# Optimization experiments

Hardware: AMD Instinct MI355X
Metric: run time of the kernel (lower is better)

The kernel has to match this reference:

```python
import jax, jax.numpy as jnp
import numpy as np
from jax import lax

BN_EPS = 1e-5


def _bn(t, g, b, m, v):
    # eval-mode BatchNorm2d over channel axis 1
    scale = (g / jnp.sqrt(v + BN_EPS))[None, :, None, None]
    return (t - m[None, :, None, None]) * scale + b[None, :, None, None]


def _conv1x1(t, w):
    # w: (out_c, in_c)
    return jnp.einsum('bchw,oc->bohw', t, w)


def setup_inputs() -> dict:
    key = jax.random.key(0)
    ks = jax.random.split(key, 8)
    B, C_in, H, W = 16, 640, 32, 32
    x = jax.random.normal(ks[0], (B, C_in, H, W), dtype=jnp.float32)

    def bn_params(k, c):
        k1, k2, k3, k4 = jax.random.split(k, 4)
        return (jax.random.normal(k1, (c,), jnp.float32) * 0.1 + 1.0,  # gamma
                jax.random.normal(k2, (c,), jnp.float32) * 0.1,        # beta
                jax.random.normal(k3, (c,), jnp.float32) * 0.1,        # running mean
                jax.random.uniform(k4, (c,), jnp.float32) + 0.5)       # running var

    bn1_g, bn1_b, bn1_m, bn1_v = bn_params(ks[1], 640)
    w_in = jax.random.normal(ks[2], (64, 640), jnp.float32) / np.sqrt(640)
    bnin_g, bnin_b, bnin_m, bnin_v = bn_params(ks[3], 64)
    w_emb = jax.random.normal(ks[4], (640, 1664), jnp.float32) / np.sqrt(1664)
    bne_g, bne_b, bne_m, bne_v = bn_params(ks[5], 640)
    w_out = jax.random.normal(ks[6], (640, 640), jnp.float32) / np.sqrt(640)
    bno_g, bno_b, bno_m, bno_v = bn_params(ks[7], 640)

    return dict(x=x,
                bn1_g=bn1_g, bn1_b=bn1_b, bn1_m=bn1_m, bn1_v=bn1_v,
                w_in=w_in, bnin_g=bnin_g, bnin_b=bnin_b, bnin_m=bnin_m, bnin_v=bnin_v,
                w_emb=w_emb, bne_g=bne_g, bne_b=bne_b, bne_m=bne_m, bne_v=bne_v,
                w_out=w_out, bno_g=bno_g, bno_b=bno_b, bno_m=bno_m, bno_v=bno_v)


def reference(x,
              bn1_g, bn1_b, bn1_m, bn1_v,
              w_in, bnin_g, bnin_b, bnin_m, bnin_v,
              w_emb, bne_g, bne_b, bne_m, bne_v,
              w_out, bno_g, bno_b, bno_m, bno_v):
    KH, KW = 5, 5
    x = jax.nn.relu(_bn(x, bn1_g, bn1_b, bn1_m, bn1_v))
    x = jax.nn.relu(_bn(_conv1x1(x, w_in), bnin_g, bnin_b, bnin_m, bnin_v))
    x0 = jax.nn.relu(x)  # second ReLU in original forward (no-op but faithful)
    # F.normalize(x, dim=1, p=2), eps=1e-12 (PyTorch default)
    norm = jnp.sqrt(jnp.sum(x0 * x0, axis=1, keepdims=True))
    identity = x0 / jnp.maximum(norm, 1e-12)
    b, c, h, w = identity.shape
    # unfold: (b, c*KH*KW, h, w), channel-major ordering matches torch Unfold
    patches = lax.conv_general_dilated_patches(
        identity, (KH, KW), (1, 1), ((2, 2), (2, 2)))
    corr = patches.reshape(b, c, KH * KW, h, w) * identity[:, :, None, :, :]
    corr = corr.reshape(b, c * KH * KW, h, w)
    # featureL2Norm: sqrt(sum(x^2, 1) + 1e-6)
    gs = corr / jnp.sqrt(jnp.sum(corr * corr, axis=1, keepdims=True) + 1e-6)
    feat = jnp.concatenate([identity, gs], axis=1)  # (b, 1664, h, w)
    e = jax.nn.relu(_bn(_conv1x1(feat, w_emb), bne_g, bne_b, bne_m, bne_v))
    out = _bn(_conv1x1(e, w_out), bno_g, bno_b, bno_m, bno_v)
    # dropout in eval mode = identity
    return out
```

## Files before the change

kernel.cpp:

```cpp
#include <hip/hip_runtime.h>
#include <math.h>

#define BN_EPS 1e-5f

using short8  = __attribute__((ext_vector_type(8))) short;
using f32x16  = __attribute__((ext_vector_type(16))) float;


__device__ __forceinline__ float bflo(unsigned u) { return __uint_as_float(u << 16); }
__device__ __forceinline__ float bfhi(unsigned u) { return __uint_as_float(u & 0xffff0000u); }

__device__ __forceinline__ unsigned bf16_rne(float f) {
    unsigned u = __float_as_uint(f);
    return (u + 0x7fffu + ((u >> 16) & 1u)) >> 16;
}
__device__ __forceinline__ unsigned pack_bf16(float lo, float hi) {
    return bf16_rne(lo) | (bf16_rne(hi) << 16);
}
__device__ __forceinline__ unsigned pk_hu(float lo, float hi) {
    unsigned a = __float_as_uint(lo) + 0x8000u;
    unsigned b = __float_as_uint(hi) + 0x8000u;
    return __builtin_amdgcn_perm(b, a, 0x07060302u);
}
__device__ __forceinline__ unsigned pmul_fast(unsigned a, unsigned b) {
    return pk_hu(bflo(a) * bflo(b), bfhi(a) * bfhi(b));
}

__global__ __launch_bounds__(256)
void k_prepAll(const float* __restrict__ g1, const float* __restrict__ b1,
               const float* __restrict__ m1, const float* __restrict__ v1,
               const float* __restrict__ w_in,
               const float* __restrict__ gi, const float* __restrict__ bi,
               const float* __restrict__ mi, const float* __restrict__ vi,
               const float* __restrict__ w_emb,
               const float* __restrict__ ge, const float* __restrict__ be,
               const float* __restrict__ me, const float* __restrict__ ve,
               const float* __restrict__ w_out,
               const float* __restrict__ go, const float* __restrict__ bo,
               const float* __restrict__ mo, const float* __restrict__ vo,
               float* __restrict__ s1, float* __restrict__ b1c,
               float* __restrict__ biasI, float* __restrict__ biasE, float* __restrict__ biasO,
               unsigned* __restrict__ wIt, unsigned* __restrict__ wEt, unsigned* __restrict__ wOt)
{
    __shared__ float row[1664];
    const int tid = threadIdx.x;

    if (blockIdx.x < 640) {
        const int oc = blockIdx.x;
#pragma unroll
        for (int it = 0; it < 2; it++) {
            int u = it * 256 + tid;
            if (u < 416)
                ((float4*)row)[u] = ((const float4*)&w_emb[(size_t)oc * 1664])[u];
        }
        __syncthreads();
        if (tid < 208) {
            int kc = tid >> 2, kh = (tid >> 1) & 1, ksub = tid & 1;
            int k0 = kc * 32 + kh * 16 + ksub * 8;
            float sc = ge[oc] * rsqrtf(ve[oc] + BN_EPS);
            float v[8];
#pragma unroll
            for (int j = 0; j < 8; j++) {
                int kgp = k0 + j;
                int orig;
                if (kgp < 64) orig = kgp;
                else { int t = kgp - 64; orig = 64 + (t & 63) * 25 + (t >> 6); }
                v[j] = row[orig] * sc;
            }
            int mt = oc >> 7, mf = (oc >> 5) & 3;
            int idx = (mt * 52 + kc) * 512 + (mf * 2 + kh) * 64 + ksub * 32 + (oc & 31);
            ((uint4*)wEt)[idx] = make_uint4(pack_bf16(v[0], v[1]), pack_bf16(v[2], v[3]),
                                            pack_bf16(v[4], v[5]), pack_bf16(v[6], v[7]));
        }
        return;
    }

    int i = (blockIdx.x - 640) * 256 + tid;

    if (i < 640) {
        float s = g1[i] * rsqrtf(v1[i] + BN_EPS);
        s1[i] = s; b1c[i] = b1[i] - m1[i] * s;
    } else if (i < 704) {
        int c = i - 640;
        float s = gi[c] * rsqrtf(vi[c] + BN_EPS);
        biasI[c] = bi[c] - mi[c] * s;
    } else if (i < 1344) {
        int c = i - 704;
        float s = ge[c] * rsqrtf(ve[c] + BN_EPS);
        biasE[c] = be[c] - me[c] * s;
    } else if (i < 1984) {
        int c = i - 1344;
        float s = go[c] * rsqrtf(vo[c] + BN_EPS);
        biasO[c] = bo[c] - mo[c] * s;
    }

    if (i >= 2048 && i < 7168) {
        int u = i - 2048;
        int kc = u >> 8, w = u & 255;
        int mf = w >> 7, kh = (w >> 6) & 1, sl = w & 63;
        int oc = mf * 32 + (sl & 31);
        int k0 = kc * 32 + kh * 16 + (sl >> 5) * 8;
        float sc = gi[oc] * rsqrtf(vi[oc] + BN_EPS);
        unsigned d[4];
#pragma unroll
        for (int q = 0; q < 4; q++)
            d[q] = pack_bf16(w_in[oc * 640 + k0 + 2 * q] * sc,
                             w_in[oc * 640 + k0 + 2 * q + 1] * sc);
        ((uint4*)wIt)[u] = make_uint4(d[0], d[1], d[2], d[3]);
    }

    if (i >= 8192 && i < 59392) {
        int u = i - 8192;
        int ci = u >> 9, w = u & 511;
        int mt = ci / 20, kc = ci - mt * 20;
        int mf = w >> 7, kh = (w >> 6) & 1, sl = w & 63;
        int oc = mt * 128 + mf * 32 + (sl & 31);
        int k0 = kc * 32 + kh * 16 + (sl >> 5) * 8;
        float sc = go[oc] * rsqrtf(vo[oc] + BN_EPS);
        unsigned d[4];
#pragma unroll
        for (int q = 0; q < 4; q++)
            d[q] = pack_bf16(w_out[oc * 640 + k0 + 2 * q] * sc,
                             w_out[oc * 640 + k0 + 2 * q + 1] * sc);
        ((uint4*)wOt)[u] = make_uint4(d[0], d[1], d[2], d[3]);
    }
}

__global__ __launch_bounds__(512, 1)
void k_identity(const float* __restrict__ x,
                const float* __restrict__ s1, const float* __restrict__ b1c,
                const unsigned* __restrict__ wIt, const float* __restrict__ biasI,
                unsigned* __restrict__ ident)
{
    __shared__ short smem[2][4096];
    __shared__ float Tpart[64 * 65];
    __shared__ float T[64 * 68];
    __shared__ float inv[64];

    const int tid  = threadIdx.x;
    const int half = tid >> 8;
    const int t    = tid & 255;
    const int l = t & 63, wv = t >> 6;
    const int mf = wv >> 1, nf = wv & 1;
    const int p0 = blockIdx.x * 64;
    const int b = p0 >> 10, hw0 = p0 & 1023;

    f32x16 acc;
#pragma unroll
    for (int r = 0; r < 16; r++) acc[r] = 0.f;

    for (int i = 0; i < 10; i++) {
        const int kc = half * 10 + i;
        uint4 av = ((const uint4*)wIt)[kc * 256 + t];
        int bnf = t >> 7, bkh = (t >> 6) & 1, sl = t & 63;
        int px = bnf * 32 + (sl & 31);
        int ch0 = kc * 32 + bkh * 16 + (sl >> 5) * 8;
        float4 sA = *(const float4*)&s1[ch0], sB = *(const float4*)&s1[ch0 + 4];
        float4 bA = *(const float4*)&b1c[ch0], bB = *(const float4*)&b1c[ch0 + 4];
        float vv[8];
        const float* xp = &x[((size_t)b * 640 + ch0) * 1024 + hw0 + px];
        vv[0] = fmaxf(fmaf(xp[0], sA.x, bA.x), 0.f);
        vv[1] = fmaxf(fmaf(xp[1024], sA.y, bA.y), 0.f);
        vv[2] = fmaxf(fmaf(xp[2048], sA.z, bA.z), 0.f);
        vv[3] = fmaxf(fmaf(xp[3072], sA.w, bA.w), 0.f);
        vv[4] = fmaxf(fmaf(xp[4096], sB.x, bB.x), 0.f);
        vv[5] = fmaxf(fmaf(xp[5120], sB.y, bB.y), 0.f);
        vv[6] = fmaxf(fmaf(xp[6144], sB.z, bB.z), 0.f);
        vv[7] = fmaxf(fmaf(xp[7168], sB.w, bB.w), 0.f);
        uint4 bvpk = make_uint4(pack_bf16(vv[0], vv[1]), pack_bf16(vv[2], vv[3]),
                                pack_bf16(vv[4], vv[5]), pack_bf16(vv[6], vv[7]));
        __syncthreads();
        ((uint4*)smem[half])[t] = av;
        ((uint4*)(smem[half] + 2048))[t] = bvpk;
        __syncthreads();
#pragma unroll
        for (int kh = 0; kh < 2; kh++) {
            short8 a  = *(const short8*)&smem[half][((mf * 2 + kh) * 64 + l) * 8];
            short8 bb = *(const short8*)&smem[half][2048 + ((nf * 2 + kh) * 64 + l) * 8];
            acc = __builtin_amdgcn_mfma_f32_32x32x16_bf16(a, bb, acc, 0, 0, 0);
        }
    }
    if (half == 1) {
#pragma unroll
        for (int r = 0; r < 16; r++) {
            int m = mf * 32 + (r & 3) + 8 * (r >> 2) + 4 * (l >> 5);
            int px = nf * 32 + (l & 31);
            Tpart[px * 65 + m] = acc[r];
        }
    }
    __syncthreads();
    if (half == 0) {
#pragma unroll
        for (int r = 0; r < 16; r++) {
            int m = mf * 32 + (r & 3) + 8 * (r >> 2) + 4 * (l >> 5);
            int px = nf * 32 + (l & 31);
            float v = acc[r] + Tpart[px * 65 + m];
            T[px * 68 + m] = fmaxf(v + biasI[m], 0.f);
        }
    }
    __syncthreads();
    if (tid < 64) {
        float sum = 0.f;
#pragma unroll 8
        for (int c = 0; c < 64; c++) { float v = T[tid * 68 + c]; sum = fmaf(v, v, sum); }
        inv[tid] = 1.f / fmaxf(sqrtf(sum), 1e-12f);
    }
    __syncthreads();
    {
        int px = tid >> 3, q = tid & 7;
        float iv = inv[px];
        unsigned d[4];
#pragma unroll
        for (int t2 = 0; t2 < 4; t2++)
            d[t2] = pack_bf16(T[px * 68 + q * 8 + 2 * t2] * iv,
                              T[px * 68 + q * 8 + 2 * t2 + 1] * iv);
        *(uint4*)&ident[(size_t)(p0 + px) * 32 + q * 4] = make_uint4(d[0], d[1], d[2], d[3]);
    }
}

#define FS_SLAB 0
#define FS_CTRS 15552
__global__ __launch_bounds__(512, 1)
void k_feat(const unsigned* __restrict__ ident, unsigned* __restrict__ featC, int ptBase)
{
    __shared__ short smem[20160];
    __shared__ float invDs[64];

    const int tid = threadIdx.x;
    const int pt = ptBase + blockIdx.x;
    const int b = pt >> 4, r0 = (pt & 15) * 2;

#pragma unroll
    for (int it = 0; it < 4; it++) {
        int u = it * 512 + tid;
        if (u < 1728) {
            int spx = u >> 3, q = u & 7;
            int sr = spx / 36, sc = spx - sr * 36;
            int r = r0 + sr - 2, c = sc - 2;
            uint4 v = make_uint4(0u, 0u, 0u, 0u);
            if (r >= 0 && r < 32 && c >= 0 && c < 32)
                v = *(const uint4*)&ident[((size_t)(b * 1024 + r * 32 + c) * 64 + q * 8) / 2];
            *(uint4*)&smem[FS_SLAB + spx * 72 + q * 8] = v;
        }
    }
    __syncthreads();

    {
        int px = tid >> 3, part = tid & 7;
        int rh = px >> 5, rw = px & 31;
        float ctr[8];
        const unsigned* cp = (const unsigned*)&smem[FS_SLAB + ((rh + 2) * 36 + rw + 2) * 72 + part * 8];
#pragma unroll
        for (int d = 0; d < 4; d++) { ctr[2 * d] = bflo(cp[d]); ctr[2 * d + 1] = bfhi(cp[d]); }
        float sum = 0.f;
#pragma unroll
        for (int k = 0; k < 25; k++) {
            const int kh = k / 5, kw = k % 5;
            const unsigned* nb = (const unsigned*)&smem[FS_SLAB + ((rh + kh) * 36 + rw + kw) * 72 + part * 8];
#pragma unroll
            for (int d = 0; d < 4; d++) {
                float q0 = bflo(nb[d]) * ctr[2 * d];
                float q1 = bfhi(nb[d]) * ctr[2 * d + 1];
                sum = fmaf(q0, q0, sum); sum = fmaf(q1, q1, sum);
            }
        }
        sum += __shfl_xor(sum, 1);
        sum += __shfl_xor(sum, 2);
        sum += __shfl_xor(sum, 4);
        if (part == 0) invDs[px] = rsqrtf(sum + 1e-6f);
    }
    __syncthreads();

    {
        int px = tid >> 3, q = tid & 7;
        int spx = ((px >> 5) + 2) * 36 + (px & 31) + 2;
        const unsigned* src = (const unsigned*)&smem[FS_SLAB + spx * 72 + q * 8];
        float iv = invDs[px];
        unsigned d[4];
#pragma unroll
        for (int dd = 0; dd < 4; dd++)
            d[dd] = pk_hu(bflo(src[dd]) * iv, bfhi(src[dd]) * iv);
        *(uint4*)&smem[FS_CTRS + px * 72 + q * 8] = make_uint4(d[0], d[1], d[2], d[3]);
    }
    __syncthreads();

    const int t = tid & 255;
    const int hf = t >> 7, bkh = (t >> 6) & 1, sl = t & 63;
    const int pxl = hf * 32 + (sl & 31);
    const int cl = bkh * 16 + (sl >> 5) * 8;
    const int spxC = (hf + 2) * 36 + (sl & 31) + 2;
    const int kcH = tid >> 8;
    uint4* dst = (uint4*)featC + (size_t)blockIdx.x * 52 * 256 + t;

    for (int it = 0; it < 26; it++) {
        int kc = it * 2 + kcH;
        uint4 f;
        if (kc < 2) {
            f = *(const uint4*)&smem[FS_SLAB + spxC * 72 + kc * 32 + cl];
        } else {
            int idx = kc - 2;
            int ksp = idx >> 1;
            int cb = (idx & 1) * 32 + cl;
            int kho = ksp / 5, kwo = ksp - kho * 5;
            int spx = (hf + kho) * 36 + (sl & 31) + kwo;
            const unsigned* nb = (const unsigned*)&smem[FS_SLAB + spx * 72 + cb];
            const unsigned* ct = (const unsigned*)&smem[FS_CTRS + pxl * 72 + cb];
            f = make_uint4(pmul_fast(nb[0], ct[0]), pmul_fast(nb[1], ct[1]),
                           pmul_fast(nb[2], ct[2]), pmul_fast(nb[3], ct[3]));
        }
        dst[kc * 256] = f;
    }
}

__global__ __launch_bounds__(128, 3)
void k_emb(const unsigned* __restrict__ featC, const unsigned* __restrict__ wEt,
           const float* __restrict__ biasE, unsigned* __restrict__ eG, int ntBase)
{
    __shared__ short Ep[64 * 136];

    const int tid = threadIdx.x;
    const int l = tid & 63, mh = tid >> 6;
    const int ntL = blockIdx.x, mt = blockIdx.y;

    f32x16 acc[2][2];
#pragma unroll
    for (int i = 0; i < 2; i++)
#pragma unroll
        for (int j = 0; j < 2; j++)
#pragma unroll
            for (int r = 0; r < 16; r++) acc[i][j][r] = 0.f;

    const uint4* A = (const uint4*)wEt + (size_t)(mt * 52) * 512;
    const uint4* B = (const uint4*)featC + (size_t)ntL * 52 * 256;

    for (int kc = 0; kc < 52; kc++) {
        uint4 av[2][2], bv[2][2];
#pragma unroll
        for (int mi = 0; mi < 2; mi++)
#pragma unroll
            for (int kh = 0; kh < 2; kh++)
                av[mi][kh] = A[(size_t)kc * 512 + (((mh * 2 + mi) * 2 + kh) << 6) + l];
#pragma unroll
        for (int ni = 0; ni < 2; ni++)
#pragma unroll
            for (int kh = 0; kh < 2; kh++)
                bv[ni][kh] = B[(size_t)kc * 256 + (ni << 7) + (kh << 6) + l];
#pragma unroll
        for (int kh = 0; kh < 2; kh++) {
            acc[0][0] = __builtin_amdgcn_mfma_f32_32x32x16_bf16(*(short8*)&av[0][kh], *(short8*)&bv[0][kh], acc[0][0], 0, 0, 0);
            acc[0][1] = __builtin_amdgcn_mfma_f32_32x32x16_bf16(*(short8*)&av[0][kh], *(short8*)&bv[1][kh], acc[0][1], 0, 0, 0);
            acc[1][0] = __builtin_amdgcn_mfma_f32_32x32x16_bf16(*(short8*)&av[1][kh], *(short8*)&bv[0][kh], acc[1][0], 0, 0, 0);
            acc[1][1] = __builtin_amdgcn_mfma_f32_32x32x16_bf16(*(short8*)&av[1][kh], *(short8*)&bv[1][kh], acc[1][1], 0, 0, 0);
        }
    }

#pragma unroll
    for (int mi = 0; mi < 2; mi++)
#pragma unroll
        for (int ni = 0; ni < 2; ni++) {
            int px = ni * 32 + (l & 31);
#pragma unroll
            for (int r = 0; r < 16; r += 2) {
                int m = (mh * 2 + mi) * 32 + (r & 3) + 8 * (r >> 2) + 4 * (l >> 5);
                float v0 = fmaxf(acc[mi][ni][r] + biasE[mt * 128 + m], 0.f);
                float v1 = fmaxf(acc[mi][ni][r + 1] + biasE[mt * 128 + m + 1], 0.f);
                *(unsigned*)&Ep[px * 136 + m] = pack_bf16(v0, v1);
            }
        }
    __syncthreads();
    const int ptg = ntBase + ntL;
#pragma unroll
    for (int it = 0; it < 8; it++) {
        int w = it * 128 + tid;
        int oct = w >> 6, pxl = w & 63;
        uint4 v = *(const uint4*)&Ep[pxl * 136 + oct * 8];
        int kcp = mt * 4 + (oct >> 2);
        int bkh = (oct >> 1) & 1, ksub = oct & 1;
        int hf = pxl >> 5, sl2 = ksub * 32 + (pxl & 31);
        ((uint4*)eG)[((size_t)ptg * 20 + kcp) * 256 + (hf << 7) + (bkh << 6) + sl2] = v;
    }
}

__global__ __launch_bounds__(128, 3)
void k_out(const unsigned* __restrict__ eG, const unsigned* __restrict__ wOt,
           const float* __restrict__ biasO, float* __restrict__ out)
{
    const int tid = threadIdx.x;
    const int l = tid & 63, mh = tid >> 6;
    const int nt = blockIdx.x, mt = blockIdx.y;
    const int p0 = nt * 64;
    const int b = p0 >> 10, hw0 = p0 & 1023;

    f32x16 acc[2][2];
#pragma unroll
    for (int i = 0; i < 2; i++)
#pragma unroll
        for (int j = 0; j < 2; j++)
#pragma unroll
            for (int r = 0; r < 16; r++) acc[i][j][r] = 0.f;

    const uint4* A = (const uint4*)wOt + (size_t)(mt * 20) * 512;
    const uint4* B = (const uint4*)eG + (size_t)nt * 20 * 256;

    for (int kc = 0; kc < 20; kc++) {
        uint4 av[2][2], bv[2][2];
#pragma unroll
        for (int mi = 0; mi < 2; mi++)
#pragma unroll
            for (int kh = 0; kh < 2; kh++)
                av[mi][kh] = A[(size_t)kc * 512 + (((mh * 2 + mi) * 2 + kh) << 6) + l];
#pragma unroll
        for (int ni = 0; ni < 2; ni++)
#pragma unroll
            for (int kh = 0; kh < 2; kh++)
                bv[ni][kh] = B[(size_t)kc * 256 + (ni << 7) + (kh << 6) + l];
#pragma unroll
        for (int kh = 0; kh < 2; kh++) {
            acc[0][0] = __builtin_amdgcn_mfma_f32_32x32x16_bf16(*(short8*)&av[0][kh], *(short8*)&bv[0][kh], acc[0][0], 0, 0, 0);
            acc[0][1] = __builtin_amdgcn_mfma_f32_32x32x16_bf16(*(short8*)&av[0][kh], *(short8*)&bv[1][kh], acc[0][1], 0, 0, 0);
            acc[1][0] = __builtin_amdgcn_mfma_f32_32x32x16_bf16(*(short8*)&av[1][kh], *(short8*)&bv[0][kh], acc[1][0], 0, 0, 0);
            acc[1][1] = __builtin_amdgcn_mfma_f32_32x32x16_bf16(*(short8*)&av[1][kh], *(short8*)&bv[1][kh], acc[1][1], 0, 0, 0);
        }
    }
#pragma unroll
    for (int mi = 0; mi < 2; mi++)
#pragma unroll
        for (int ni = 0; ni < 2; ni++) {
            int pxl = ni * 32 + (l & 31);
#pragma unroll
            for (int r = 0; r < 16; r++) {
                int oc = mt * 128 + (mh * 2 + mi) * 32 + (r & 3) + 8 * (r >> 2) + 4 * (l >> 5);
                out[((size_t)b * 640 + oc) * 1024 + hw0 + pxl] = acc[mi][ni][r] + biasO[oc];
            }
        }
}

extern "C" void kernel_launch(void* const* d_in, const int* in_sizes, int n_in,
                              void* d_out, int out_size, void* d_ws, size_t ws_size,
                              hipStream_t stream)
{
    const float* x    = (const float*)d_in[0];
    const float* g1   = (const float*)d_in[1];
    const float* b1   = (const float*)d_in[2];
    const float* m1   = (const float*)d_in[3];
    const float* v1   = (const float*)d_in[4];
    const float* w_in = (const float*)d_in[5];
    const float* gi   = (const float*)d_in[6];
    const float* bi   = (const float*)d_in[7];
    const float* mi   = (const float*)d_in[8];
    const float* vi   = (const float*)d_in[9];
    const float* w_emb= (const float*)d_in[10];
    const float* ge   = (const float*)d_in[11];
    const float* be   = (const float*)d_in[12];
    const float* me   = (const float*)d_in[13];
    const float* ve   = (const float*)d_in[14];
    const float* w_out= (const float*)d_in[15];
    const float* go   = (const float*)d_in[16];
    const float* bo   = (const float*)d_in[17];
    const float* mo   = (const float*)d_in[18];
    const float* vo   = (const float*)d_in[19];

    char* ws = (char*)d_ws;
    float*    s1    = (float*)(ws + 0);
    float*    b1c   = (float*)(ws + 2560);
    float*    biasI = (float*)(ws + 5120);
    float*    biasE = (float*)(ws + 5376);
    float*    biasO = (float*)(ws + 7936);
    unsigned* wIt   = (unsigned*)(ws + 16384);
    unsigned* wOt   = (unsigned*)(ws + 98304);
    unsigned* wEt   = (unsigned*)(ws + 917504);
    unsigned* ident = (unsigned*)(ws + 3047424);
    unsigned* eG    = (unsigned*)(ws + 5144576);
    float*    out   = (float*)d_out;

    const size_t featFullOff = 26116096ull;
    const size_t featFullBytes = 256ull * 52 * 256 * 16;

    k_prepAll<<<872, 256, 0, stream>>>(g1, b1, m1, v1, w_in, gi, bi, mi, vi,
                                       w_emb, ge, be, me, ve, w_out, go, bo, mo, vo,
                                       s1, b1c, biasI, biasE, biasO, wIt, wEt, wOt);
    k_identity<<<256, 512, 0, stream>>>(x, s1, b1c, wIt, biasI, ident);

    if (ws_size >= featFullOff + featFullBytes) {
        unsigned* featC = (unsigned*)(ws + featFullOff);
        k_feat<<<256, 512, 0, stream>>>(ident, featC, 0);
        k_emb<<<dim3(256, 5), 128, 0, stream>>>(featC, wEt, biasE, eG, 0);
    } else {
        unsigned* featC = (unsigned*)(ws + 16384);
        for (int c = 0; c < 64; c++) {
            k_feat<<<4, 512, 0, stream>>>(ident, featC, c * 4);
            k_emb<<<dim3(4, 5), 128, 0, stream>>>(featC, wEt, biasE, eG, c * 4);
        }
        k_prepAll<<<872, 256, 0, stream>>>(g1, b1, m1, v1, w_in, gi, bi, mi, vi,
                                           w_emb, ge, be, me, ve, w_out, go, bo, mo, vo,
                                           s1, b1c, biasI, biasE, biasO, wIt, wEt, wOt);
    }
    k_out<<<dim3(256, 5), 128, 0, stream>>>(eG, wOt, biasO, out);
}
```

Before: 221.0 us.

## Split K across two wave pairs in emb and out GEMMs with LDS reduction

Both the embedding and output GEMM kernels now run 256 threads per block. Each pair of waves handles half of the K dimension, and the two partial accumulators are combined through a shared-memory float buffer before the bias, ReLU and store. The goal is to shorten each block's serial K loop and put more waves in flight to hide global-load latency, since both kernels load operands straight from global memory with no prefetching. In exchange each block uses 32KB of LDS, needs extra syncs and a reduction pass, and the epilogue now packs bf16 from fp32 LDS.

```diff
diff --git a/kernel.cpp b/kernel.cpp
--- a/kernel.cpp
+++ b/kernel.cpp
@@ -312,14 +312,17 @@
     }
 }
 
-__global__ __launch_bounds__(128, 3)
+__global__ __launch_bounds__(256, 4)
 void k_emb(const unsigned* __restrict__ featC, const unsigned* __restrict__ wEt,
            const float* __restrict__ biasE, unsigned* __restrict__ eG, int ntBase)
 {
-    __shared__ short Ep[64 * 136];
+    __shared__ float R[128 * 64];
 
     const int tid = threadIdx.x;
-    const int l = tid & 63, mh = tid >> 6;
+    const int l = tid & 63;
+    const int wv = tid >> 6;
+    const int mh = wv & 1;
+    const int half = wv >> 1;
     const int ntL = blockIdx.x, mt = blockIdx.y;
 
     f32x16 acc[2][2];
@@ -330,10 +333,10 @@
 #pragma unroll
             for (int r = 0; r < 16; r++) acc[i][j][r] = 0.f;
 
-    const uint4* A = (const uint4*)wEt + (size_t)(mt * 52) * 512;
-    const uint4* B = (const uint4*)featC + (size_t)ntL * 52 * 256;
-
-    for (int kc = 0; kc < 52; kc++) {
+    const uint4* A = (const uint4*)wEt + ((size_t)(mt * 52) + half * 26) * 512;
+    const uint4* B = (const uint4*)featC + ((size_t)ntL * 52 + half * 26) * 256;
+
+    for (int kc = 0; kc < 26; kc++) {
         uint4 av[2][2], bv[2][2];
 #pragma unroll
         for (int mi = 0; mi < 2; mi++)
@@ -354,39 +357,65 @@
         }
     }
 
-#pragma unroll
-    for (int mi = 0; mi < 2; mi++)
-#pragma unroll
-        for (int ni = 0; ni < 2; ni++) {
-            int px = ni * 32 + (l & 31);
-#pragma unroll
-            for (int r = 0; r < 16; r += 2) {
-                int m = (mh * 2 + mi) * 32 + (r & 3) + 8 * (r >> 2) + 4 * (l >> 5);
-                float v0 = fmaxf(acc[mi][ni][r] + biasE[mt * 128 + m], 0.f);
-                float v1 = fmaxf(acc[mi][ni][r + 1] + biasE[mt * 128 + m + 1], 0.f);
-                *(unsigned*)&Ep[px * 136 + m] = pack_bf16(v0, v1);
+    if (half == 1) {
+#pragma unroll
+        for (int mi = 0; mi < 2; mi++)
+#pragma unroll
+            for (int ni = 0; ni < 2; ni++) {
+                int px = ni * 32 + (l & 31);
+#pragma unroll
+                for (int r = 0; r < 16; r++) {
+                    int m = (mh * 2 + mi) * 32 + (r & 3) + 8 * (r >> 2) + 4 * (l >> 5);
+                    R[m * 64 + px] = acc[mi][ni][r];
+                }
             }
-        }
-    __syncthreads();
+    }
+    __syncthreads();
+    if (half == 0) {
+#pragma unroll
+        for (int mi = 0; mi < 2; mi++)
+#pragma unroll
+            for (int ni = 0; ni < 2; ni++) {
+                int px = ni * 32 + (l & 31);
+#pragma unroll
+                for (int r = 0; r < 16; r++) {
+                    int m = (mh * 2 + mi) * 32 + (r & 3) + 8 * (r >> 2) + 4 * (l >> 5);
+                    int idx = m * 64 + px;
+                    R[idx] = fmaxf(acc[mi][ni][r] + R[idx] + biasE[mt * 128 + m], 0.f);
+                }
+            }
+    }
+    __syncthreads();
+
     const int ptg = ntBase + ntL;
 #pragma unroll
-    for (int it = 0; it < 8; it++) {
-        int w = it * 128 + tid;
+    for (int it = 0; it < 4; it++) {
+        int w = it * 256 + tid;
         int oct = w >> 6, pxl = w & 63;
-        uint4 v = *(const uint4*)&Ep[pxl * 136 + oct * 8];
+        const float* rp = &R[(oct * 8) * 64 + pxl];
+        unsigned d[4];
+#pragma unroll
+        for (int q = 0; q < 4; q++)
+            d[q] = pack_bf16(rp[(2 * q) * 64], rp[(2 * q + 1) * 64]);
         int kcp = mt * 4 + (oct >> 2);
         int bkh = (oct >> 1) & 1, ksub = oct & 1;
         int hf = pxl >> 5, sl2 = ksub * 32 + (pxl & 31);
-        ((uint4*)eG)[((size_t)ptg * 20 + kcp) * 256 + (hf << 7) + (bkh << 6) + sl2] = v;
-    }
-}
-
-__global__ __launch_bounds__(128, 3)
+        ((uint4*)eG)[((size_t)ptg * 20 + kcp) * 256 + (hf << 7) + (bkh << 6) + sl2] =
+            make_uint4(d[0], d[1], d[2], d[3]);
+    }
+}
+
+__global__ __launch_bounds__(256, 4)
 void k_out(const unsigned* __restrict__ eG, const unsigned* __restrict__ wOt,
            const float* __restrict__ biasO, float* __restrict__ out)
 {
+    __shared__ float R[128 * 64];
+
     const int tid = threadIdx.x;
-    const int l = tid & 63, mh = tid >> 6;
+    const int l = tid & 63;
+    const int wv = tid >> 6;
+    const int mh = wv & 1;
+    const int half = wv >> 1;
     const int nt = blockIdx.x, mt = blockIdx.y;
     const int p0 = nt * 64;
     const int b = p0 >> 10, hw0 = p0 & 1023;
@@ -399,10 +428,10 @@
 #pragma unroll
             for (int r = 0; r < 16; r++) acc[i][j][r] = 0.f;
 
-    const uint4* A = (const uint4*)wOt + (size_t)(mt * 20) * 512;
-    const uint4* B = (const uint4*)eG + (size_t)nt * 20 * 256;
-
-    for (int kc = 0; kc < 20; kc++) {
+    const uint4* A = (const uint4*)wOt + ((size_t)(mt * 20) + half * 10) * 512;
+    const uint4* B = (const uint4*)eG + ((size_t)nt * 20 + half * 10) * 256;
+
+    for (int kc = 0; kc < 10; kc++) {
         uint4 av[2][2], bv[2][2];
 #pragma unroll
         for (int mi = 0; mi < 2; mi++)
@@ -422,17 +451,36 @@
             acc[1][1] = __builtin_amdgcn_mfma_f32_32x32x16_bf16(*(short8*)&av[1][kh], *(short8*)&bv[1][kh], acc[1][1], 0, 0, 0);
         }
     }
-#pragma unroll
-    for (int mi = 0; mi < 2; mi++)
-#pragma unroll
-        for (int ni = 0; ni < 2; ni++) {
-            int pxl = ni * 32 + (l & 31);
-#pragma unroll
-            for (int r = 0; r < 16; r++) {
-                int oc = mt * 128 + (mh * 2 + mi) * 32 + (r & 3) + 8 * (r >> 2) + 4 * (l >> 5);
-                out[((size_t)b * 640 + oc) * 1024 + hw0 + pxl] = acc[mi][ni][r] + biasO[oc];
+
+    if (half == 1) {
+#pragma unroll
+        for (int mi = 0; mi < 2; mi++)
+#pragma unroll
+            for (int ni = 0; ni < 2; ni++) {
+                int px = ni * 32 + (l & 31);
+#pragma unroll
+                for (int r = 0; r < 16; r++) {
+                    int m = (mh * 2 + mi) * 32 + (r & 3) + 8 * (r >> 2) + 4 * (l >> 5);
+                    R[m * 64 + px] = acc[mi][ni][r];
+                }
             }
-        }
+    }
+    __syncthreads();
+    if (half == 0) {
+#pragma unroll
+        for (int mi = 0; mi < 2; mi++)
+#pragma unroll
+            for (int ni = 0; ni < 2; ni++) {
+                int pxl = ni * 32 + (l & 31);
+#pragma unroll
+                for (int r = 0; r < 16; r++) {
+                    int m = (mh * 2 + mi) * 32 + (r & 3) + 8 * (r >> 2) + 4 * (l >> 5);
+                    int oc = mt * 128 + m;
+                    out[((size_t)b * 640 + oc) * 1024 + hw0 + pxl] =
+                        acc[mi][ni][r] + R[m * 64 + pxl] + biasO[oc];
+                }
+            }
+    }
 }
 
 extern "C" void kernel_launch(void* const* d_in, const int* in_sizes, int n_in,
@@ -484,16 +532,16 @@
     if (ws_size >= featFullOff + featFullBytes) {
         unsigned* featC = (unsigned*)(ws + featFullOff);
         k_feat<<<256, 512, 0, stream>>>(ident, featC, 0);
-        k_emb<<<dim3(256, 5), 128, 0, stream>>>(featC, wEt, biasE, eG, 0);
+        k_emb<<<dim3(256, 5), 256, 0, stream>>>(featC, wEt, biasE, eG, 0);
     } else {
         unsigned* featC = (unsigned*)(ws + 16384);
         for (int c = 0; c < 64; c++) {
             k_feat<<<4, 512, 0, stream>>>(ident, featC, c * 4);
-            k_emb<<<dim3(4, 5), 128, 0, stream>>>(featC, wEt, biasE, eG, c * 4);
+            k_emb<<<dim3(4, 5), 256, 0, stream>>>(featC, wEt, biasE, eG, c * 4);
         }
         k_prepAll<<<872, 256, 0, stream>>>(g1, b1, m1, v1, w_in, gi, bi, mi, vi,
                                            w_emb, ge, be, me, ve, w_out, go, bo, mo, vo,
                                            s1, b1c, biasI, biasE, biasO, wIt, wEt, wOt);
     }
-    k_out<<<dim3(256, 5), 128, 0, stream>>>(eG, wOt, biasO, out);
-}
+    k_out<<<dim3(256, 5), 256, 0, stream>>>(eG, wOt, biasO, out);
+}
```

After: 223.5 us. About the same (+1.1%).

## Merge output-channel tiles into one 640-thread block sharing LDS-staged activations

Applied to the files above, without the earlier changes.

k_emb and k_out now launch one 640-thread block per 64-pixel tile covering all 640 output channels, instead of five 128-thread blocks per tile. Each block stages the activation (B) operand in double-buffered LDS, so the 10 waves share it rather than each re-reading it from global memory, and the next chunk is prefetched while MFMAs run. The k_emb epilogue now writes bf16 results straight into eG's layout, dropping the LDS transpose and its barrier. In exchange the grid shrinks to 256 large blocks, at most one per CU, which cuts occupancy and latency hiding. Each k-step also adds a block-wide barrier.

```diff
diff --git a/kernel.cpp b/kernel.cpp
--- a/kernel.cpp
+++ b/kernel.cpp
@@ -312,116 +312,167 @@
     }
 }
 
-__global__ __launch_bounds__(128, 3)
+__global__ __launch_bounds__(640, 1)
 void k_emb(const unsigned* __restrict__ featC, const unsigned* __restrict__ wEt,
            const float* __restrict__ biasE, unsigned* __restrict__ eG, int ntBase)
 {
-    __shared__ short Ep[64 * 136];
+    __shared__ char lds[2][16384];
 
     const int tid = threadIdx.x;
-    const int l = tid & 63, mh = tid >> 6;
-    const int ntL = blockIdx.x, mt = blockIdx.y;
-
-    f32x16 acc[2][2];
-#pragma unroll
-    for (int i = 0; i < 2; i++)
-#pragma unroll
-        for (int j = 0; j < 2; j++)
-#pragma unroll
-            for (int r = 0; r < 16; r++) acc[i][j][r] = 0.f;
+    const int l = tid & 63;
+    const int w = tid >> 6;
+    const int mt = w >> 1, mf0 = (w & 1) * 2;
+    const int ntL = blockIdx.x;
 
     const uint4* A = (const uint4*)wEt + (size_t)(mt * 52) * 512;
     const uint4* B = (const uint4*)featC + (size_t)ntL * 52 * 256;
 
-    for (int kc = 0; kc < 52; kc++) {
-        uint4 av[2][2], bv[2][2];
-#pragma unroll
-        for (int mi = 0; mi < 2; mi++)
-#pragma unroll
-            for (int kh = 0; kh < 2; kh++)
-                av[mi][kh] = A[(size_t)kc * 512 + (((mh * 2 + mi) * 2 + kh) << 6) + l];
-#pragma unroll
-        for (int ni = 0; ni < 2; ni++)
-#pragma unroll
-            for (int kh = 0; kh < 2; kh++)
-                bv[ni][kh] = B[(size_t)kc * 256 + (ni << 7) + (kh << 6) + l];
-#pragma unroll
-        for (int kh = 0; kh < 2; kh++) {
-            acc[0][0] = __builtin_amdgcn_mfma_f32_32x32x16_bf16(*(short8*)&av[0][kh], *(short8*)&bv[0][kh], acc[0][0], 0, 0, 0);
-            acc[0][1] = __builtin_amdgcn_mfma_f32_32x32x16_bf16(*(short8*)&av[0][kh], *(short8*)&bv[1][kh], acc[0][1], 0, 0, 0);
-            acc[1][0] = __builtin_amdgcn_mfma_f32_32x32x16_bf16(*(short8*)&av[1][kh], *(short8*)&bv[0][kh], acc[1][0], 0, 0, 0);
-            acc[1][1] = __builtin_amdgcn_mfma_f32_32x32x16_bf16(*(short8*)&av[1][kh], *(short8*)&bv[1][kh], acc[1][1], 0, 0, 0);
-        }
-    }
-
-#pragma unroll
-    for (int mi = 0; mi < 2; mi++)
+    const int u0 = tid;
+    const int u1 = tid + 640;
+    const bool has2 = (tid < 384);
+
+    f32x16 acc[2][2];
+#pragma unroll
+    for (int i = 0; i < 2; i++)
+#pragma unroll
+        for (int j = 0; j < 2; j++)
+#pragma unroll
+            for (int r = 0; r < 16; r++) acc[i][j][r] = 0.f;
+
+    uint4 s0 = B[u0];
+    uint4 s1;
+    if (has2) s1 = B[u1];
+    *(uint4*)&lds[0][u0 * 16] = s0;
+    if (has2) *(uint4*)&lds[0][u1 * 16] = s1;
+    __syncthreads();
+
+    for (int c = 0; c < 13; c++) {
+        const int cur = c & 1, nxt = cur ^ 1;
+        if (c < 12) {
+            s0 = B[(c + 1) * 1024 + u0];
+            if (has2) s1 = B[(c + 1) * 1024 + u1];
+        }
+#pragma unroll
+        for (int kcL = 0; kcL < 4; kcL++) {
+            const int kc = c * 4 + kcL;
+            uint4 av[2][2], bv[2][2];
+#pragma unroll
+            for (int mi = 0; mi < 2; mi++)
+#pragma unroll
+                for (int kh = 0; kh < 2; kh++)
+                    av[mi][kh] = A[(size_t)kc * 512 + (((mf0 + mi) * 2 + kh) << 6) + l];
+#pragma unroll
+            for (int ni = 0; ni < 2; ni++)
+#pragma unroll
+                for (int kh = 0; kh < 2; kh++)
+                    bv[ni][kh] = *(const uint4*)&lds[cur][(kcL * 256 + (ni << 7) + (kh << 6) + l) * 16];
+#pragma unroll
+            for (int kh = 0; kh < 2; kh++) {
+                acc[0][0] = __builtin_amdgcn_mfma_f32_32x32x16_bf16(*(short8*)&av[0][kh], *(short8*)&bv[0][kh], acc[0][0], 0, 0, 0);
+                acc[0][1] = __builtin_amdgcn_mfma_f32_32x32x16_bf16(*(short8*)&av[0][kh], *(short8*)&bv[1][kh], acc[0][1], 0, 0, 0);
+                acc[1][0] = __builtin_amdgcn_mfma_f32_32x32x16_bf16(*(short8*)&av[1][kh], *(short8*)&bv[0][kh], acc[1][0], 0, 0, 0);
+                acc[1][1] = __builtin_amdgcn_mfma_f32_32x32x16_bf16(*(short8*)&av[1][kh], *(short8*)&bv[1][kh], acc[1][1], 0, 0, 0);
+            }
+        }
+        if (c < 12) {
+            *(uint4*)&lds[nxt][u0 * 16] = s0;
+            if (has2) *(uint4*)&lds[nxt][u1 * 16] = s1;
+        }
+        __syncthreads();
+    }
+
+    const int ptg = ntBase + ntL;
+#pragma unroll
+    for (int mi = 0; mi < 2; mi++) {
+        const size_t kbase = ((size_t)ptg * 20 + (w * 2 + mi)) * 256;
 #pragma unroll
         for (int ni = 0; ni < 2; ni++) {
-            int px = ni * 32 + (l & 31);
-#pragma unroll
-            for (int r = 0; r < 16; r += 2) {
-                int m = (mh * 2 + mi) * 32 + (r & 3) + 8 * (r >> 2) + 4 * (l >> 5);
-                float v0 = fmaxf(acc[mi][ni][r] + biasE[mt * 128 + m], 0.f);
-                float v1 = fmaxf(acc[mi][ni][r + 1] + biasE[mt * 128 + m + 1], 0.f);
-                *(unsigned*)&Ep[px * 136 + m] = pack_bf16(v0, v1);
+#pragma unroll
+            for (int rg = 0; rg < 4; rg++) {
+                int ocb = w * 64 + mi * 32 + 8 * rg + 4 * (l >> 5);
+                float4 bb = *(const float4*)&biasE[ocb];
+                unsigned d0 = pack_bf16(fmaxf(acc[mi][ni][rg * 4 + 0] + bb.x, 0.f),
+                                        fmaxf(acc[mi][ni][rg * 4 + 1] + bb.y, 0.f));
+                unsigned d1 = pack_bf16(fmaxf(acc[mi][ni][rg * 4 + 2] + bb.z, 0.f),
+                                        fmaxf(acc[mi][ni][rg * 4 + 3] + bb.w, 0.f));
+                size_t unit = kbase + (ni << 7) + ((rg >> 1) << 6) + ((rg & 1) << 5) + (l & 31);
+                ((uint2*)eG)[unit * 2 + (l >> 5)] = make_uint2(d0, d1);
             }
         }
-    __syncthreads();
-    const int ptg = ntBase + ntL;
-#pragma unroll
-    for (int it = 0; it < 8; it++) {
-        int w = it * 128 + tid;
-        int oct = w >> 6, pxl = w & 63;
-        uint4 v = *(const uint4*)&Ep[pxl * 136 + oct * 8];
-        int kcp = mt * 4 + (oct >> 2);
-        int bkh = (oct >> 1) & 1, ksub = oct & 1;
-        int hf = pxl >> 5, sl2 = ksub * 32 + (pxl & 31);
-        ((uint4*)eG)[((size_t)ptg * 20 + kcp) * 256 + (hf << 7) + (bkh << 6) + sl2] = v;
-    }
-}
-
-__global__ __launch_bounds__(128, 3)
+    }
+}
+
+__global__ __launch_bounds__(640, 1)
 void k_out(const unsigned* __restrict__ eG, const unsigned* __restrict__ wOt,
            const float* __restrict__ biasO, float* __restrict__ out)
 {
+    __shared__ char lds[2][16384];
+
     const int tid = threadIdx.x;
-    const int l = tid & 63, mh = tid >> 6;
-    const int nt = blockIdx.x, mt = blockIdx.y;
+    const int l = tid & 63;
+    const int w = tid >> 6;
+    const int mt = w >> 1, mf0 = (w & 1) * 2;
+    const int nt = blockIdx.x;
     const int p0 = nt * 64;
     const int b = p0 >> 10, hw0 = p0 & 1023;
 
-    f32x16 acc[2][2];
-#pragma unroll
-    for (int i = 0; i < 2; i++)
-#pragma unroll
-        for (int j = 0; j < 2; j++)
-#pragma unroll
-            for (int r = 0; r < 16; r++) acc[i][j][r] = 0.f;
-
     const uint4* A = (const uint4*)wOt + (size_t)(mt * 20) * 512;
     const uint4* B = (const uint4*)eG + (size_t)nt * 20 * 256;
 
-    for (int kc = 0; kc < 20; kc++) {
-        uint4 av[2][2], bv[2][2];
-#pragma unroll
-        for (int mi = 0; mi < 2; mi++)
-#pragma unroll
-            for (int kh = 0; kh < 2; kh++)
-                av[mi][kh] = A[(size_t)kc * 512 + (((mh * 2 + mi) * 2 + kh) << 6) + l];
-#pragma unroll
-        for (int ni = 0; ni < 2; ni++)
-#pragma unroll
-            for (int kh = 0; kh < 2; kh++)
-                bv[ni][kh] = B[(size_t)kc * 256 + (ni << 7) + (kh << 6) + l];
-#pragma unroll
-        for (int kh = 0; kh < 2; kh++) {
-            acc[0][0] = __builtin_amdgcn_mfma_f32_32x32x16_bf16(*(short8*)&av[0][kh], *(short8*)&bv[0][kh], acc[0][0], 0, 0, 0);
-            acc[0][1] = __builtin_amdgcn_mfma_f32_32x32x16_bf16(*(short8*)&av[0][kh], *(short8*)&bv[1][kh], acc[0][1], 0, 0, 0);
-            acc[1][0] = __builtin_amdgcn_mfma_f32_32x32x16_bf16(*(short8*)&av[1][kh], *(short8*)&bv[0][kh], acc[1][0], 0, 0, 0);
-            acc[1][1] = __builtin_amdgcn_mfma_f32_32x32x16_bf16(*(short8*)&av[1][kh], *(short8*)&bv[1][kh], acc[1][1], 0, 0, 0);
-        }
-    }
+    const int u0 = tid;
+    const int u1 = tid + 640;
+    const bool has2 = (tid < 384);
+
+    f32x16 acc[2][2];
+#pragma unroll
+    for (int i = 0; i < 2; i++)
+#pragma unroll
+        for (int j = 0; j < 2; j++)
+#pragma unroll
+            for (int r = 0; r < 16; r++) acc[i][j][r] = 0.f;
+
+    uint4 s0 = B[u0];
+    uint4 s1;
+    if (has2) s1 = B[u1];
+    *(uint4*)&lds[0][u0 * 16] = s0;
+    if (has2) *(uint4*)&lds[0][u1 * 16] = s1;
+    __syncthreads();
+
+    for (int c = 0; c < 5; c++) {
+        const int cur = c & 1, nxt = cur ^ 1;
+        if (c < 4) {
+            s0 = B[(c + 1) * 1024 + u0];
+            if (has2) s1 = B[(c + 1) * 1024 + u1];
+        }
+#pragma unroll
+        for (int kcL = 0; kcL < 4; kcL++) {
+            const int kc = c * 4 + kcL;
+            uint4 av[2][2], bv[2][2];
+#pragma unroll
+            for (int mi = 0; mi < 2; mi++)
+#pragma unroll
+                for (int kh = 0; kh < 2; kh++)
+                    av[mi][kh] = A[(size_t)kc * 512 + (((mf0 + mi) * 2 + kh) << 6) + l];
+#pragma unroll
+            for (int ni = 0; ni < 2; ni++)
+#pragma unroll
+                for (int kh = 0; kh < 2; kh++)
+                    bv[ni][kh] = *(const uint4*)&lds[cur][(kcL * 256 + (ni << 7) + (kh << 6) + l) * 16];
+#pragma unroll
+            for (int kh = 0; kh < 2; kh++) {
+                acc[0][0] = __builtin_amdgcn_mfma_f32_32x32x16_bf16(*(short8*)&av[0][kh], *(short8*)&bv[0][kh], acc[0][0], 0, 0, 0);
+                acc[0][1] = __builtin_amdgcn_mfma_f32_32x32x16_bf16(*(short8*)&av[0][kh], *(short8*)&bv[1][kh], acc[0][1], 0, 0, 0);
+                acc[1][0] = __builtin_amdgcn_mfma_f32_32x32x16_bf16(*(short8*)&av[1][kh], *(short8*)&bv[0][kh], acc[1][0], 0, 0, 0);
+                acc[1][1] = __builtin_amdgcn_mfma_f32_32x32x16_bf16(*(short8*)&av[1][kh], *(short8*)&bv[1][kh], acc[1][1], 0, 0, 0);
+            }
+        }
+        if (c < 4) {
+            *(uint4*)&lds[nxt][u0 * 16] = s0;
+            if (has2) *(uint4*)&lds[nxt][u1 * 16] = s1;
+        }
+        __syncthreads();
+    }
+
 #pragma unroll
     for (int mi = 0; mi < 2; mi++)
 #pragma unroll
@@ -429,7 +480,7 @@
             int pxl = ni * 32 + (l & 31);
 #pragma unroll
             for (int r = 0; r < 16; r++) {
-                int oc = mt * 128 + (mh * 2 + mi) * 32 + (r & 3) + 8 * (r >> 2) + 4 * (l >> 5);
+                int oc = w * 64 + mi * 32 + (r & 3) + 8 * (r >> 2) + 4 * (l >> 5);
                 out[((size_t)b * 640 + oc) * 1024 + hw0 + pxl] = acc[mi][ni][r] + biasO[oc];
             }
         }
@@ -484,16 +535,16 @@
     if (ws_size >= featFullOff + featFullBytes) {
         unsigned* featC = (unsigned*)(ws + featFullOff);
         k_feat<<<256, 512, 0, stream>>>(ident, featC, 0);
-        k_emb<<<dim3(256, 5), 128, 0, stream>>>(featC, wEt, biasE, eG, 0);
+        k_emb<<<256, 640, 0, stream>>>(featC, wEt, biasE, eG, 0);
     } else {
         unsigned* featC = (unsigned*)(ws + 16384);
         for (int c = 0; c < 64; c++) {
             k_feat<<<4, 512, 0, stream>>>(ident, featC, c * 4);
-            k_emb<<<dim3(4, 5), 128, 0, stream>>>(featC, wEt, biasE, eG, c * 4);
+            k_emb<<<4, 640, 0, stream>>>(featC, wEt, biasE, eG, c * 4);
         }
         k_prepAll<<<872, 256, 0, stream>>>(g1, b1, m1, v1, w_in, gi, bi, mi, vi,
                                            w_emb, ge, be, me, ve, w_out, go, bo, mo, vo,
                                            s1, b1c, biasI, biasE, biasO, wIt, wEt, wOt);
     }
-    k_out<<<dim3(256, 5), 128, 0, stream>>>(eG, wOt, biasO, out);
-}
+    k_out<<<256, 640, 0, stream>>>(eG, wOt, biasO, out);
+}
```

After: 218.6 us. No clear change (-1.1%).
